# Kernel tuning notes

Measured on AMD Instinct MI355X. Metric: run time of the kernel, lower is better.

## Reference

```python
import jax, jax.numpy as jnp
import numpy as np

H_LSTM = 80          # span-encoder LSTM hidden
SPAN_DIM = 4 * H_LSTM  # 320
ADU_DIM = 256        # han_out_size
HEADS = 3
HAN_HID = 256
CTX_DIM = 200


def lstm(x, W_ih, W_hh, b, reverse=False):
    # x: [T, B, In] -> hidden states [T, B, H]; torch gate order i,f,g,o
    H = W_hh.shape[1]
    B = x.shape[1]

    def step(carry, xt):
        h, c = carry
        z = xt @ W_ih.T + h @ W_hh.T + b
        i, f, g, o = jnp.split(z, 4, axis=-1)
        c = jax.nn.sigmoid(f) * c + jax.nn.sigmoid(i) * jnp.tanh(g)
        h = jax.nn.sigmoid(o) * jnp.tanh(c)
        return (h, c), h

    init = (jnp.zeros((B, H), x.dtype), jnp.zeros((B, H), x.dtype))
    _, hs = jax.lax.scan(step, init, x, reverse=reverse)
    return hs


def span_rep(seq, spans):
    # seq [L, 2H], spans [..., 2] -> [..., 4H]
    f, bwd = seq[:, :H_LSTM], seq[:, H_LSTM:]
    i, j = spans[..., 0], spans[..., 1]
    fi1, fj = f[i - 1], f[j]
    bi, bj1 = bwd[i], bwd[j + 1]
    return jnp.concatenate([fj - fi1, bi - bj1, fi1, bj1], axis=-1)


def gat_metapath(h, src, dst, emask, W, a_l, a_r, bias):
    # single-metapath GATConv (dgl semantics): h [A, Din], W [K, Din, D]
    A = h.shape[0]
    hp = jnp.einsum('ad,kdo->ako', h, W)  # [A,K,D]
    e = jax.nn.leaky_relu(jnp.einsum('eko,ko->ek', hp[src], a_l)
                          + jnp.einsum('eko,ko->ek', hp[dst], a_r), 0.2)
    e = jnp.where(emask[:, None], e, -1e9)
    m = jax.ops.segment_max(e, dst, num_segments=A)           # [A,K]
    ex = jnp.where(emask[:, None], jnp.exp(e - m[dst]), 0.0)
    den = jax.ops.segment_sum(ex, dst, num_segments=A)
    alpha = ex / jnp.maximum(den[dst], 1e-9)                  # edge softmax per dst
    out = jax.ops.segment_sum(alpha[:, :, None] * hp[src], dst, num_segments=A)
    out = jax.nn.elu(out + bias)                              # [A,K,D]
    return out.reshape(A, -1)                                 # [A, K*D]


def attn_pool(feats, vals, mask, W1, b1, W2, b2):
    # tiny MLP -> Softmax over axis 0 over the kept (masked) set
    s = jnp.maximum(feats @ W1 + b1, 0.0) @ W2 + b2           # [N,1]
    s = jnp.where(mask[:, None], s, -1e9)
    a = jnp.where(mask[:, None], jax.nn.softmax(s, axis=0), 0.0)
    out = (a * vals).sum(0)
    return jnp.where(mask.any(), out, jnp.zeros_like(out))


def _forward(token_embed, info_scores,
             Wih_f, Whh_f, b_f, Wih_b, Whh_b, b_b,
             W_gat, a_l, a_r, b_gat, W_sem, b_sem, q_sem, W_pred, b_pred,
             W_adu1, b_adu1, W_adu2, b_adu2,
             W_inn1, b_inn1, W_inn2, b_inn2,
             W_int1, b_int1, W_int2, b_int2,
             Wih_c, Whh_c, b_c,
             comment_spans, adu_spans, adu_masks, local_masks,
             inner_src, inner_dst, inner_rel, inner_mask,
             inter_src, inter_dst, inter_rel, inter_mask):
    # bidirectional span encoder over frozen LF token embeddings
    x = token_embed.transpose(1, 0, 2)                        # [L, C, 768]
    hf = lstm(x, Wih_f, Whh_f, b_f)
    hb = lstm(x, Wih_b, Whh_b, b_b, reverse=True)
    span_enc = jnp.concatenate([hf, hb], -1).transpose(1, 0, 2)  # [C, L, 2H]

    def per_comment(seq, cspan, aspans, amask, lmask,
                    isrc, idst, irel, imask_e,
                    tsrc, tdst, trel, tmask_e, info):
        cemb = span_rep(seq, cspan)                           # [320]
        adus = span_rep(seq, aspans) * amask[:, None]         # [A, 320]
        A = adus.shape[0]
        # meta-paths: inner Attack, inner Support, inter AttackedBy(rev), inter SupportedBy(rev)
        srcs = jnp.stack([isrc, isrc, tdst, tdst])
        dsts = jnp.stack([idst, idst, tsrc, tsrc])
        masks = jnp.stack([imask_e & (irel == 0), imask_e & (irel == 1),
                           tmask_e & (trel == 0), tmask_e & (trel == 1)])
        z = jax.vmap(gat_metapath, in_axes=(None, 0, 0, 0, 0, 0, 0, 0))(
            adus, srcs, dsts, masks, W_gat, a_l, a_r, b_gat)  # [4, A, K*D]
        # semantic attention across meta-paths (masked mean over real nodes)
        w = jnp.tanh(z @ W_sem + b_sem) @ q_sem               # [4, A]
        w = (w * amask[None, :]).sum(1) / jnp.maximum(amask.sum(), 1)
        beta = jax.nn.softmax(w)                              # [4]
        zfin = jnp.einsum('m,mad->ad', beta, z)               # [A, K*D]
        adu_embeds = zfin @ W_pred + b_pred                   # [A, 256]
        # ADU attention pooling over locally-used ADUs
        feats = jnp.concatenate(
            [jnp.broadcast_to(cemb, (A, SPAN_DIM)), adu_embeds], -1)
        attended_adu = attn_pool(feats, adu_embeds, amask & lmask,
                                 W_adu1, b_adu1, W_adu2, b_adu2)

        def pair_attend(se, de, rel, me, W1, b1, W2, b2):
            # relation lut: Attack(0)->[0,1], Support(1)->[1,0]
            onehot = jnp.stack([rel, 1 - rel], -1).astype(adu_embeds.dtype)
            pe = jnp.concatenate([adu_embeds[se], adu_embeds[de], onehot], -1)  # [E,514]
            fp = jnp.concatenate(
                [jnp.broadcast_to(cemb, (pe.shape[0], SPAN_DIM)), pe], -1)
            return attn_pool(fp, pe, me, W1, b1, W2, b2)

        attended_inner = pair_attend(isrc, idst, irel, imask_e,
                                     W_inn1, b_inn1, W_inn2, b_inn2)
        # revert_inter_post_relations=True: embed = cat(emb[pair1], emb[pair0], rel)
        attended_inter = pair_attend(tdst, tsrc, trel, tmask_e,
                                     W_int1, b_int1, W_int2, b_int2)
        return jnp.concatenate([attended_adu, attended_inner, attended_inter,
                                info, cemb])                  # [1608]

    wo_ctx = jax.vmap(per_comment)(span_enc, comment_spans, adu_spans, adu_masks,
                                   local_masks, inner_src, inner_dst, inner_rel,
                                   inner_mask, inter_src, inter_dst, inter_rel,
                                   inter_mask, info_scores)   # [C, 1608]
    # comment compressor LSTM along the comment sequence (batch = 1)
    ctx = lstm(wo_ctx[:, None, :], Wih_c, Whh_c, b_c)[:, 0, :]  # [C, 200]
    return jnp.concatenate([ctx, wo_ctx], -1)                 # [C, 1808]


def setup_inputs():
    C, L, A, E, INFO = 64, 1024, 32, 48, 4
    key = jax.random.key(0)
    ks = iter(jax.random.split(key, 64))
    rng = np.random.default_rng(0)

    def u(shape):  # uniform init as in _weight_init, scaled for stability
        return jax.random.uniform(next(ks), shape, jnp.float32, -0.1, 0.1)

    token_embed = jax.random.normal(next(ks), (C, L, 768), jnp.float32)
    info_scores = jax.random.normal(next(ks), (C, INFO), jnp.float32)
    ci = rng.integers(1, L // 2, C)
    cj = rng.integers(L // 2, L - 2, C)
    comment_spans = jnp.stack([jnp.asarray(ci), jnp.asarray(cj)], 1).astype(jnp.int32)
    ai = rng.integers(1, L - 40, (C, A))
    adu_spans = jnp.stack([jnp.asarray(ai), jnp.asarray(ai + rng.integers(1, 30, (C, A)))], -1).astype(jnp.int32)
    adu_masks = jnp.ones((C, A), jnp.bool_)
    local_masks = jnp.asarray(rng.integers(0, 2, (C, A)) > 0)
    ei = lambda hi, shp: jnp.asarray(rng.integers(0, hi, shp), jnp.int32)
    eb = lambda shp: jnp.asarray(rng.integers(0, 2, shp) > 0)
    inp = dict(token_embed=token_embed, info_scores=info_scores,
               comment_spans=comment_spans, adu_spans=adu_spans,
               adu_masks=adu_masks, local_masks=local_masks,
               inner_src=ei(A, (C, E)), inner_dst=ei(A, (C, E)),
               inner_rel=ei(2, (C, E)), inner_mask=eb((C, E)),
               inter_src=ei(A, (C, E)), inter_dst=ei(A, (C, E)),
               inter_rel=ei(2, (C, E)), inter_mask=eb((C, E)))
    D_WO = SPAN_DIM + ADU_DIM * 5 + 4 + INFO  # 1608
    params = dict(
        Wih_f=u((4 * H_LSTM, 768)), Whh_f=u((4 * H_LSTM, H_LSTM)), b_f=u((4 * H_LSTM,)),
        Wih_b=u((4 * H_LSTM, 768)), Whh_b=u((4 * H_LSTM, H_LSTM)), b_b=u((4 * H_LSTM,)),
        W_gat=u((4, HEADS, SPAN_DIM, HAN_HID)), a_l=u((4, HEADS, HAN_HID)),
        a_r=u((4, HEADS, HAN_HID)), b_gat=u((4, HEADS, HAN_HID)),
        W_sem=u((HEADS * HAN_HID, 128)), b_sem=u((128,)), q_sem=u((128,)),
        W_pred=u((HEADS * HAN_HID, ADU_DIM)), b_pred=u((ADU_DIM,)),
        W_adu1=u((SPAN_DIM + ADU_DIM, 16)), b_adu1=u((16,)), W_adu2=u((16, 1)), b_adu2=u((1,)),
        W_inn1=u((SPAN_DIM + 2 * ADU_DIM + 2, 16)), b_inn1=u((16,)), W_inn2=u((16, 1)), b_inn2=u((1,)),
        W_int1=u((SPAN_DIM + 2 * ADU_DIM + 2, 16)), b_int1=u((16,)), W_int2=u((16, 1)), b_int2=u((1,)),
        Wih_c=u((4 * CTX_DIM, D_WO)), Whh_c=u((4 * CTX_DIM, CTX_DIM)), b_c=u((4 * CTX_DIM,)))
    inp.update(params)
    return inp


def reference(token_embed, info_scores,
              Wih_f, Whh_f, b_f, Wih_b, Whh_b, b_b,
              W_gat, a_l, a_r, b_gat, W_sem, b_sem, q_sem, W_pred, b_pred,
              W_adu1, b_adu1, W_adu2, b_adu2,
              W_inn1, b_inn1, W_inn2, b_inn2,
              W_int1, b_int1, W_int2, b_int2,
              Wih_c, Whh_c, b_c,
              comment_spans, adu_spans, adu_masks, local_masks,
              inner_src, inner_dst, inner_rel, inner_mask,
              inter_src, inter_dst, inter_rel, inter_mask):
    return _forward(token_embed, info_scores,
                    Wih_f, Whh_f, b_f, Wih_b, Whh_b, b_b,
                    W_gat, a_l, a_r, b_gat, W_sem, b_sem, q_sem, W_pred, b_pred,
                    W_adu1, b_adu1, W_adu2, b_adu2,
                    W_inn1, b_inn1, W_inn2, b_inn2,
                    W_int1, b_int1, W_int2, b_int2,
                    Wih_c, Whh_c, b_c,
                    comment_spans, adu_spans, adu_masks, local_masks,
                    inner_src, inner_dst, inner_rel, inner_mask,
                    inter_src, inter_dst, inter_rel, inter_mask)
```

## Files before the change

### kernel.cpp

```cpp
#include <hip/hip_runtime.h>
#include <hip/hip_bf16.h>
#include <hip/hip_fp16.h>
#include <stdint.h>

typedef unsigned int u32;
typedef unsigned short u16;
typedef __attribute__((ext_vector_type(8))) short short8;
typedef __attribute__((ext_vector_type(4))) float f32x4;
typedef _Float16 half2v __attribute__((ext_vector_type(2)));

#if defined(__has_builtin)
#if __has_builtin(__builtin_amdgcn_fdot2)
#define HAVE_FDOT2 1
#endif
#endif

#define LDS_BARRIER()                                        \
  do {                                                       \
    asm volatile("s_waitcnt lgkmcnt(0)" ::: "memory");       \
    __builtin_amdgcn_s_barrier();                            \
    asm volatile("" ::: "memory");                           \
  } while (0)

__device__ __forceinline__ float bf2f_u(u32 lo16) { return __uint_as_float(lo16 << 16); }
__device__ __forceinline__ u32 f2bf_bits(float x) {
  u32 u = __float_as_uint(x);
  return (u + 0x7fffu + ((u >> 16) & 1u)) >> 16;
}
__device__ __forceinline__ u32 pk2bf_tr(float x, float y) {
  return (__float_as_uint(y) & 0xffff0000u) | (__float_as_uint(x) >> 16);
}
__device__ __forceinline__ u32 pkh(float x, float y) {
  return (u32)__half_as_ushort(__float2half(x)) |
         ((u32)__half_as_ushort(__float2half(y)) << 16);
}
__device__ __forceinline__ float dot2h(u32 w, u32 h, float acc) {
#ifdef HAVE_FDOT2
  return __builtin_amdgcn_fdot2(__builtin_bit_cast(half2v, w), __builtin_bit_cast(half2v, h),
                                acc, false);
#else
  union { u32 u; __half2 h2; } uw, uh;
  uw.u = w; uh.u = h;
  float2 wf = __half22float2(uw.h2);
  float2 hf = __half22float2(uh.h2);
  return acc + wf.x * hf.x + wf.y * hf.y;
#endif
}
__device__ __forceinline__ float sigf(float x) { return 1.0f / (1.0f + __expf(-x)); }
__device__ __forceinline__ float tanhf_fast(float x) {
  float ax = fabsf(x);
  float e = __expf(-2.0f * ax);
  float t = (1.0f - e) / (1.0f + e);
  return x < 0.0f ? -t : t;
}
__device__ __forceinline__ float eluf(float x) { return x > 0.0f ? x : __expf(x) - 1.0f; }
__device__ __forceinline__ float lreluf(float x) { return x > 0.0f ? x : 0.2f * x; }

__device__ __forceinline__ int maskmode(const void* am) { return (*(const u32*)am) > 0xFFu; }
__device__ __forceinline__ int ldmask(const void* p, int i, int mb) {
  return mb ? (int)((const unsigned char*)p)[i] : ((const int*)p)[i];
}

__global__ void k_marker(float* out) { out[0] = 12345.0f; }

__global__ __launch_bounds__(256) void k_prep(const float* __restrict__ Wgat,
                                              const float* __restrict__ al,
                                              const float* __restrict__ ar,
                                              float* __restrict__ alproj,
                                              float* __restrict__ arproj) {
  int w = blockIdx.x * 4 + (threadIdx.x >> 6);
  int lane = threadIdx.x & 63;
  if (w >= 3840) return;
  int mk = w / 320, d = w % 320;
  const float* wrow = Wgat + ((size_t)mk * 320 + d) * 256;
  const float* alp = al + mk * 256;
  const float* arp = ar + mk * 256;
  float sa = 0.f, sb = 0.f;
#pragma unroll
  for (int q = 0; q < 4; ++q) {
    int o = lane + q * 64;
    float wv = wrow[o];
    sa += wv * alp[o];
    sb += wv * arp[o];
  }
#pragma unroll
  for (int off = 32; off; off >>= 1) {
    sa += __shfl_down(sa, off, 64);
    sb += __shfl_down(sb, off, 64);
  }
  if (lane == 0) { alproj[w] = sa; arproj[w] = sb; }
}

__global__ void k_pack(const float* __restrict__ whhc, uint4* __restrict__ wt4) {
  int idx = blockIdx.x * 256 + threadIdx.x;
  if (idx >= 20000) return;
  int k4 = idx / 800, r = idx % 800;
  const float* p = whhc + r * 200 + k4 * 8;
  wt4[idx] = (uint4){pkh(p[0], p[1]), pkh(p[2], p[3]), pkh(p[4], p[5]), pkh(p[6], p[7])};
}

__global__ __launch_bounds__(256) void k_gemm_in(
    const float* __restrict__ emb, const float* __restrict__ Wf, const float* __restrict__ Wb,
    const float* __restrict__ biasf, const float* __restrict__ biasb, float* __restrict__ Z) {
  __shared__ u16 Albs[128 * 40];
  __shared__ u16 Blbs[128 * 40];
  __shared__ float bias_l[128];
  const int tid = threadIdx.x;
  const int n0 = blockIdx.x * 128;
  const int m0 = blockIdx.y * 128;

  if (tid < 128) {
    int ng = n0 + tid;
    bias_l[tid] = (ng < 320) ? biasf[ng] : biasb[ng - 320];
  }
  const int srow = tid >> 1, shalf = tid & 1;
  const float* asrc = emb + (size_t)(m0 + srow) * 768 + shalf * 16;
  const int ngb = n0 + srow;
  const float* bsrc =
      ((ngb < 320) ? (Wf + (size_t)ngb * 768) : (Wb + (size_t)(ngb - 320) * 768)) + shalf * 16;
  u32* aw = (u32*)&Albs[srow * 40 + shalf * 16];
  u32* bw = (u32*)&Blbs[srow * 40 + shalf * 16];

  const int lane = tid & 63;
  const int lr = lane & 15, sub = lane >> 4;
  const int wv = tid >> 6, wm = wv >> 1, wn = wv & 1;
  const u16* abase = &Albs[(wm * 64 + lr) * 40 + sub * 8];
  const u16* bbase = &Blbs[(wn * 64 + lr) * 40 + sub * 8];

  f32x4 acc[4][4];
#pragma unroll
  for (int i = 0; i < 4; ++i)
#pragma unroll
    for (int j = 0; j < 4; ++j) acc[i][j] = (f32x4)(0.f);

  float4 a0, a1, a2, a3, b0, b1, b2, b3;
  u32 pra[8], prb[8];
  a0 = *(const float4*)(asrc + 0); a1 = *(const float4*)(asrc + 4);
  a2 = *(const float4*)(asrc + 8); a3 = *(const float4*)(asrc + 12);
  b0 = *(const float4*)(bsrc + 0); b1 = *(const float4*)(bsrc + 4);
  b2 = *(const float4*)(bsrc + 8); b3 = *(const float4*)(bsrc + 12);
  pra[0] = pk2bf_tr(a0.x, a0.y); pra[1] = pk2bf_tr(a0.z, a0.w);
  pra[2] = pk2bf_tr(a1.x, a1.y); pra[3] = pk2bf_tr(a1.z, a1.w);
  pra[4] = pk2bf_tr(a2.x, a2.y); pra[5] = pk2bf_tr(a2.z, a2.w);
  pra[6] = pk2bf_tr(a3.x, a3.y); pra[7] = pk2bf_tr(a3.z, a3.w);
  prb[0] = pk2bf_tr(b0.x, b0.y); prb[1] = pk2bf_tr(b0.z, b0.w);
  prb[2] = pk2bf_tr(b1.x, b1.y); prb[3] = pk2bf_tr(b1.z, b1.w);
  prb[4] = pk2bf_tr(b2.x, b2.y); prb[5] = pk2bf_tr(b2.z, b2.w);
  prb[6] = pk2bf_tr(b3.x, b3.y); prb[7] = pk2bf_tr(b3.z, b3.w);

  for (int it = 0; it < 24; ++it) {
    LDS_BARRIER();
#pragma unroll
    for (int q = 0; q < 8; ++q) { aw[q] = pra[q]; bw[q] = prb[q]; }
    LDS_BARRIER();
    const bool more = (it + 1 < 24);
    if (more) {
      const int k0 = (it + 1) * 32;
      a0 = *(const float4*)(asrc + k0); a1 = *(const float4*)(asrc + k0 + 4);
      a2 = *(const float4*)(asrc + k0 + 8); a3 = *(const float4*)(asrc + k0 + 12);
      b0 = *(const float4*)(bsrc + k0); b1 = *(const float4*)(bsrc + k0 + 4);
      b2 = *(const float4*)(bsrc + k0 + 8); b3 = *(const float4*)(bsrc + k0 + 12);
    }
    short8 bfr[4];
#pragma unroll
    for (int nf = 0; nf < 4; ++nf) bfr[nf] = *(const short8*)(bbase + nf * 640);
#pragma unroll
    for (int mf = 0; mf < 4; ++mf) {
      short8 af = *(const short8*)(abase + mf * 640);
#pragma unroll
      for (int nf = 0; nf < 4; ++nf)
        acc[mf][nf] = __builtin_amdgcn_mfma_f32_16x16x32_bf16(af, bfr[nf], acc[mf][nf], 0, 0, 0);
    }
    if (more) {
      pra[0] = pk2bf_tr(a0.x, a0.y); pra[1] = pk2bf_tr(a0.z, a0.w);
      pra[2] = pk2bf_tr(a1.x, a1.y); pra[3] = pk2bf_tr(a1.z, a1.w);
      pra[4] = pk2bf_tr(a2.x, a2.y); pra[5] = pk2bf_tr(a2.z, a2.w);
      pra[6] = pk2bf_tr(a3.x, a3.y); pra[7] = pk2bf_tr(a3.z, a3.w);
      prb[0] = pk2bf_tr(b0.x, b0.y); prb[1] = pk2bf_tr(b0.z, b0.w);
      prb[2] = pk2bf_tr(b1.x, b1.y); prb[3] = pk2bf_tr(b1.z, b1.w);
      prb[4] = pk2bf_tr(b2.x, b2.y); prb[5] = pk2bf_tr(b2.z, b2.w);
      prb[6] = pk2bf_tr(b3.x, b3.y); prb[7] = pk2bf_tr(b3.z, b3.w);
    }
  }
#pragma unroll
  for (int mf = 0; mf < 4; ++mf) {
#pragma unroll
    for (int nf = 0; nf < 4; ++nf) {
      int col = wn * 64 + nf * 16 + lr;
      float bias = bias_l[col];
      size_t mrow = (size_t)m0 + wm * 64 + mf * 16 + sub * 4;
#pragma unroll
      for (int j = 0; j < 4; ++j)
        Z[(mrow + j) * 640 + n0 + col] = acc[mf][nf][j] + bias;
    }
  }
}

__global__ __launch_bounds__(320, 1) void k_lstm_tok(const float* __restrict__ Z,
                                                     const float* __restrict__ Whhf,
                                                     const float* __restrict__ Whhb,
                                                     float* __restrict__ hf,
                                                     float* __restrict__ hb) {
  __shared__ uint2 wq[20 * 320];
  __shared__ alignas(16) u32 hpk[40];
  __shared__ float zbuf[320];
  const int tid = threadIdx.x;
  const int c = blockIdx.x >> 1;
  const int dir = blockIdx.x & 1;
  const float* Whh = dir ? Whhb : Whhf;
  float* hout = dir ? hb : hf;

  for (int idx = tid; idx < 20 * 320; idx += 320) {
    int k4 = idx / 320, r = idx % 320;
    const float* p = Whh + (size_t)r * 80 + k4 * 4;
    wq[idx] = (uint2){pkh(p[0], p[1]), pkh(p[2], p[3])};
  }
  if (tid < 40) hpk[tid] = 0;
  __syncthreads();

  const int j = tid;
  const bool isG = (j >= 160) && (j < 240);
  const uint2* wcol = wq + j;
  uint2 wv0 = wcol[0], wv1 = wcol[320], wv2 = wcol[640], wv3 = wcol[960];
  uint2 wv4 = wcol[1280], wv5 = wcol[1600], wv6 = wcol[1920], wv7 = wcol[2240];
  uint2 wv8 = wcol[2560], wv9 = wcol[2880], wv10 = wcol[3200], wv11 = wcol[3520];
  uint2 wv12 = wcol[3840], wv13 = wcol[4160], wv14 = wcol[4480], wv15 = wcol[4800];
  uint2 wv16 = wcol[5120], wv17 = wcol[5440], wv18 = wcol[5760], wv19 = wcol[6080];

  const int sgn = dir ? -1 : 1;
  const int t0 = dir ? 1023 : 0;
  const float* zb = Z + (size_t)c * 1024 * 640 + dir * 320 + j;
  float zc = zb[(size_t)t0 * 640];
  float zn = zb[(size_t)(t0 + sgn) * 640];
  float cst = 0.f;

  for (int t = 0; t < 1024; ++t) {
    const int tt = t0 + sgn * t;
    float zp = 0.f;
    if (t + 2 < 1024) zp = zb[(size_t)(t0 + sgn * (t + 2)) * 640];
    float a0 = zc, a1 = 0.f, a2 = 0.f, a3 = 0.f;
    {
      uint4 h0 = *(const uint4*)&hpk[0];
      a0 = dot2h(wv0.x, h0.x, a0); a1 = dot2h(wv0.y, h0.y, a1);
      a2 = dot2h(wv1.x, h0.z, a2); a3 = dot2h(wv1.y, h0.w, a3);
      uint4 h1 = *(const uint4*)&hpk[4];
      a0 = dot2h(wv2.x, h1.x, a0); a1 = dot2h(wv2.y, h1.y, a1);
      a2 = dot2h(wv3.x, h1.z, a2); a3 = dot2h(wv3.y, h1.w, a3);
      uint4 h2 = *(const uint4*)&hpk[8];
      a0 = dot2h(wv4.x, h2.x, a0); a1 = dot2h(wv4.y, h2.y, a1);
      a2 = dot2h(wv5.x, h2.z, a2); a3 = dot2h(wv5.y, h2.w, a3);
      uint4 h3 = *(const uint4*)&hpk[12];
      a0 = dot2h(wv6.x, h3.x, a0); a1 = dot2h(wv6.y, h3.y, a1);
      a2 = dot2h(wv7.x, h3.z, a2); a3 = dot2h(wv7.y, h3.w, a3);
      uint4 h4 = *(const uint4*)&hpk[16];
      a0 = dot2h(wv8.x, h4.x, a0); a1 = dot2h(wv8.y, h4.y, a1);
      a2 = dot2h(wv9.x, h4.z, a2); a3 = dot2h(wv9.y, h4.w, a3);
      uint4 h5 = *(const uint4*)&hpk[20];
      a0 = dot2h(wv10.x, h5.x, a0); a1 = dot2h(wv10.y, h5.y, a1);
      a2 = dot2h(wv11.x, h5.z, a2); a3 = dot2h(wv11.y, h5.w, a3);
      uint4 h6 = *(const uint4*)&hpk[24];
      a0 = dot2h(wv12.x, h6.x, a0); a1 = dot2h(wv12.y, h6.y, a1);
      a2 = dot2h(wv13.x, h6.z, a2); a3 = dot2h(wv13.y, h6.w, a3);
      uint4 h7 = *(const uint4*)&hpk[28];
      a0 = dot2h(wv14.x, h7.x, a0); a1 = dot2h(wv14.y, h7.y, a1);
      a2 = dot2h(wv15.x, h7.z, a2); a3 = dot2h(wv15.y, h7.w, a3);
      uint4 h8 = *(const uint4*)&hpk[32];
      a0 = dot2h(wv16.x, h8.x, a0); a1 = dot2h(wv16.y, h8.y, a1);
      a2 = dot2h(wv17.x, h8.z, a2); a3 = dot2h(wv17.y, h8.w, a3);
      uint4 h9 = *(const uint4*)&hpk[36];
      a0 = dot2h(wv18.x, h9.x, a0); a1 = dot2h(wv18.y, h9.y, a1);
      a2 = dot2h(wv19.x, h9.z, a2); a3 = dot2h(wv19.y, h9.w, a3);
    }
    float zr = (a0 + a1) + (a2 + a3);
    zbuf[j] = isG ? tanhf_fast(zr) : sigf(zr);
    LDS_BARRIER();
    if (j < 80) {
      float iv = zbuf[j];
      float fv = zbuf[80 + j];
      float gv = zbuf[160 + j];
      float ov = zbuf[240 + j];
      cst = fv * cst + iv * gv;
      float h = ov * tanhf_fast(cst);
      ((u16*)hpk)[j] = (u16)__half_as_ushort(__float2half(h));
      hout[((size_t)c * 1024 + tt) * 80 + j] = h;
    }
    zc = zn; zn = zp;
    LDS_BARRIER();
  }
}

__device__ __forceinline__ float span_val(const float* __restrict__ hf,
                                          const float* __restrict__ hb, int c, int i, int j,
                                          int d) {
  size_t base = (size_t)c * 1024 * 80;
  if (d < 80) return hf[base + (size_t)j * 80 + d] - hf[base + (size_t)(i - 1) * 80 + d];
  if (d < 160) return hb[base + (size_t)i * 80 + (d - 80)] - hb[base + (size_t)(j + 1) * 80 + (d - 80)];
  if (d < 240) return hf[base + (size_t)(i - 1) * 80 + (d - 160)];
  return hb[base + (size_t)(j + 1) * 80 + (d - 240)];
}

__global__ __launch_bounds__(256) void k_span(const float* __restrict__ hf,
                                              const float* __restrict__ hb,
                                              const int* __restrict__ cspan,
                                              const int* __restrict__ aspan,
                                              const void* __restrict__ amask,
                                              float* __restrict__ adus, float* __restrict__ cembo) {
  const int c = blockIdx.x, tid = threadIdx.x;
  const int mb = maskmode(amask);
  int ci = cspan[c * 2], cj = cspan[c * 2 + 1];
  for (int d = tid; d < 320; d += 256) cembo[c * 320 + d] = span_val(hf, hb, c, ci, cj, d);
  for (int idx = tid; idx < 32 * 320; idx += 256) {
    int a = idx / 320, d = idx % 320;
    float v = 0.f;
    if (ldmask(amask, c * 32 + a, mb)) {
      int ai = aspan[(c * 32 + a) * 2], aj = aspan[(c * 32 + a) * 2 + 1];
      v = span_val(hf, hb, c, ai, aj, d);
    }
    adus[(size_t)c * 10240 + idx] = v;
  }
}

__global__ __launch_bounds__(256) void k_gat(
    const float* __restrict__ adus_ws, const float* __restrict__ alproj,
    const float* __restrict__ arproj, const float* __restrict__ Wgat,
    const float* __restrict__ bgat, const int* __restrict__ isrc, const int* __restrict__ idst,
    const int* __restrict__ irel, const void* __restrict__ imask, const int* __restrict__ tsrc,
    const int* __restrict__ tdst, const int* __restrict__ trel, const void* __restrict__ tmask,
    const void* __restrict__ amdet, float* __restrict__ zgat) {
  __shared__ float adus_l[32][321];
  __shared__ float Wst[16][64];
  __shared__ float hp_t[32][66];
  __shared__ float sl_l[96], sr_l[96];
  __shared__ float e_l[144], alpha_l[144], mx_l[96], den_l[96];
  __shared__ int src_l[48], dst_l[48], valid_l[48];
  const int c = blockIdx.x >> 2, m = blockIdx.x & 3;
  const int tid = threadIdx.x;
  const int mb = maskmode(amdet);

  if (tid < 48) {
    int e = tid, s, d, r, mk;
    if (m < 2) {
      s = isrc[c * 48 + e]; d = idst[c * 48 + e]; r = irel[c * 48 + e];
      mk = ldmask(imask, c * 48 + e, mb);
    } else {
      s = tdst[c * 48 + e]; d = tsrc[c * 48 + e]; r = trel[c * 48 + e];
      mk = ldmask(tmask, c * 48 + e, mb);
    }
    src_l[e] = s; dst_l[e] = d; valid_l[e] = (mk != 0) && (r == (m & 1));
  }
  for (int idx = tid; idx < 32 * 320; idx += 256)
    adus_l[idx / 320][idx % 320] = adus_ws[(size_t)c * 10240 + idx];
  __syncthreads();

  if (tid < 96) {
    int a = tid & 31, k = tid >> 5;
    const float* alp = alproj + (m * 3 + k) * 320;
    const float* arp = arproj + (m * 3 + k) * 320;
    float sa = 0.f, sb = 0.f;
    for (int d = 0; d < 320; ++d) {
      float v = adus_l[a][d];
      sa += v * alp[d];
      sb += v * arp[d];
    }
    sl_l[a * 3 + k] = sa;
    sr_l[a * 3 + k] = sb;
  }
  __syncthreads();
  if (tid < 144) {
    int e = tid % 48, k = tid / 48;
    float v = -1e30f;
    if (valid_l[e]) v = lreluf(sl_l[src_l[e] * 3 + k] + sr_l[dst_l[e] * 3 + k]);
    e_l[e * 3 + k] = v;
  }
  __syncthreads();
  if (tid < 96) {
    int a = tid & 31, k = tid >> 5;
    float mx = -1e30f;
    for (int e = 0; e < 48; ++e)
      if (valid_l[e] && dst_l[e] == a) mx = fmaxf(mx, e_l[e * 3 + k]);
    float den = 0.f;
    for (int e = 0; e < 48; ++e)
      if (valid_l[e] && dst_l[e] == a) den += __expf(e_l[e * 3 + k] - mx);
    mx_l[a * 3 + k] = mx;
    den_l[a * 3 + k] = den;
  }
  __syncthreads();
  if (tid < 144) {
    int e = tid % 48, k = tid / 48;
    float v = 0.f;
    if (valid_l[e]) {
      int d = dst_l[e];
      v = __expf(e_l[e * 3 + k] - mx_l[d * 3 + k]) / fmaxf(den_l[d * 3 + k], 1e-9f);
    }
    alpha_l[e * 3 + k] = v;
  }
  __syncthreads();

  const int ag = tid >> 3, og = tid & 7;
  const int dd_ = tid >> 4, oq_ = (tid & 15) * 4;
  for (int k = 0; k < 3; ++k) {
    for (int ot = 0; ot < 4; ++ot) {
      float acc[8];
#pragma unroll
      for (int i = 0; i < 8; ++i) acc[i] = 0.f;
      float4 pref = *(const float4*)(Wgat + ((size_t)((m * 3 + k) * 320 + dd_)) * 256 + ot * 64 + oq_);
      for (int dt = 0; dt < 320; dt += 16) {
        Wst[dd_][oq_ + 0] = pref.x;
        Wst[dd_][oq_ + 1] = pref.y;
        Wst[dd_][oq_ + 2] = pref.z;
        Wst[dd_][oq_ + 3] = pref.w;
        __syncthreads();
        if (dt + 16 < 320)
          pref = *(const float4*)(Wgat +
                                  ((size_t)((m * 3 + k) * 320 + dt + 16 + dd_)) * 256 + ot * 64 + oq_);
#pragma unroll
        for (int dd = 0; dd < 16; ++dd) {
          float av = adus_l[ag][dt + dd];
          const float4 w0 = *(const float4*)(&Wst[dd][og * 8]);
          const float4 w1 = *(const float4*)(&Wst[dd][og * 8 + 4]);
          acc[0] += av * w0.x; acc[1] += av * w0.y; acc[2] += av * w0.z; acc[3] += av * w0.w;
          acc[4] += av * w1.x; acc[5] += av * w1.y; acc[6] += av * w1.z; acc[7] += av * w1.w;
        }
        __syncthreads();
      }
#pragma unroll
      for (int i = 0; i < 8; ++i) hp_t[ag][og * 8 + i] = acc[i];
      __syncthreads();
      float oacc[8];
#pragma unroll
      for (int i = 0; i < 8; ++i) oacc[i] = 0.f;
      for (int e = 0; e < 48; ++e) {
        if (valid_l[e] && dst_l[e] == ag) {
          float alv = alpha_l[e * 3 + k];
          int s = src_l[e];
#pragma unroll
          for (int i = 0; i < 8; ++i) oacc[i] += alv * hp_t[s][og * 8 + i];
        }
      }
#pragma unroll
      for (int i = 0; i < 8; ++i) {
        int o = ot * 64 + og * 8 + i;
        float v = eluf(oacc[i] + bgat[(m * 3 + k) * 256 + o]);
        zgat[((size_t)(c * 4 + m) * 32 + ag) * 768 + k * 256 + o] = v;
      }
      __syncthreads();
    }
  }
}

__global__ __launch_bounds__(256) void k_sem(const float* __restrict__ zgat,
                                             const float* __restrict__ Wsem,
                                             const float* __restrict__ bsem,
                                             const float* __restrict__ qsem,
                                             const void* __restrict__ amask,
                                             float* __restrict__ wsem) {
  __shared__ float Wst[64][128];
  __shared__ float zl[32][64];
  __shared__ float wred[256];
  __shared__ float war[32];
  const int c = blockIdx.x >> 2, m = blockIdx.x & 3;
  const int tid = threadIdx.x;
  const int mb = maskmode(amask);
  const int a = tid >> 3, hg = tid & 7;
  float acc[16];
#pragma unroll
  for (int i = 0; i < 16; ++i) acc[i] = 0.f;
  const float* zbase = zgat + (size_t)(c * 4 + m) * 32 * 768;
  for (int jt = 0; jt < 768; jt += 64) {
    for (int l = 0; l < 8; ++l) {
      int f4 = l * 256 + tid;
      int row = f4 >> 5, c4 = (f4 & 31) * 4;
      *(float4*)&Wst[row][c4] = *(const float4*)(Wsem + (size_t)(jt + row) * 128 + c4);
    }
    for (int l = 0; l < 2; ++l) {
      int f4 = l * 256 + tid;
      int row = f4 >> 4, c4 = (f4 & 15) * 4;
      *(float4*)&zl[row][c4] = *(const float4*)(zbase + (size_t)row * 768 + jt + c4);
    }
    __syncthreads();
    for (int j = 0; j < 64; ++j) {
      float zv = zl[a][j];
      const float* wp = &Wst[j][hg * 16];
#pragma unroll
      for (int i = 0; i < 16; ++i) acc[i] += zv * wp[i];
    }
    __syncthreads();
  }
  float wp_ = 0.f;
#pragma unroll
  for (int i = 0; i < 16; ++i) {
    int h = hg * 16 + i;
    wp_ += tanhf_fast(acc[i] + bsem[h]) * qsem[h];
  }
  wred[tid] = wp_;
  __syncthreads();
  if (tid < 32) {
    float s = 0.f;
    for (int q = 0; q < 8; ++q) s += wred[tid * 8 + q];
    war[tid] = s;
  }
  __syncthreads();
  if (tid == 0) {
    float s = 0.f;
    int cnt = 0;
    for (int aa = 0; aa < 32; ++aa)
      if (ldmask(amask, c * 32 + aa, mb)) { s += war[aa]; cnt++; }
    wsem[c * 4 + m] = s / (float)(cnt > 1 ? cnt : 1);
  }
}

__global__ __launch_bounds__(256) void k_comment(
    const float* __restrict__ zgat, const float* __restrict__ wsem,
    const float* __restrict__ cemb_ws, const float* __restrict__ Wpred,
    const float* __restrict__ bpred, const float* __restrict__ Wadu1,
    const float* __restrict__ badu1, const float* __restrict__ Wadu2,
    const float* __restrict__ badu2, const float* __restrict__ Winn1,
    const float* __restrict__ binn1, const float* __restrict__ Winn2,
    const float* __restrict__ binn2, const float* __restrict__ Wint1,
    const float* __restrict__ bint1, const float* __restrict__ Wint2,
    const float* __restrict__ bint2, const float* __restrict__ info,
    const void* __restrict__ amask, const void* __restrict__ lmask,
    const int* __restrict__ isrc, const int* __restrict__ idst,
    const int* __restrict__ irel, const void* __restrict__ imask, const int* __restrict__ tsrc,
    const int* __restrict__ tdst, const int* __restrict__ trel, const void* __restrict__ tmask,
    float* __restrict__ woctx, float* __restrict__ dout) {
  __shared__ float zf[32][133];
  __shared__ float ae[32][257];
  __shared__ float wbuf[13344];
  __shared__ float cemb_l[320];
  __shared__ float beta_l[4];
  __shared__ float pred_l[48][16];
  __shared__ float sE[48], alE[48];
  __shared__ int seL[48], deL[48], relL[48], mskL[48];
  __shared__ float wredA[256];
  __shared__ float sA[32], alA[32];
  __shared__ int mskA[32];
  const int c = blockIdx.x, tid = threadIdx.x;
  const int mb = maskmode(amask);

  if (tid == 0) {
    float w0 = wsem[c * 4], w1 = wsem[c * 4 + 1], w2 = wsem[c * 4 + 2], w3 = wsem[c * 4 + 3];
    float mx = fmaxf(fmaxf(w0, w1), fmaxf(w2, w3));
    float e0 = __expf(w0 - mx), e1 = __expf(w1 - mx), e2 = __expf(w2 - mx), e3 = __expf(w3 - mx);
    float s = e0 + e1 + e2 + e3;
    beta_l[0] = e0 / s; beta_l[1] = e1 / s; beta_l[2] = e2 / s; beta_l[3] = e3 / s;
  }
  for (int d = tid; d < 320; d += 256) cemb_l[d] = cemb_ws[c * 320 + d];
  __syncthreads();

  const int ag = tid >> 5;
  const int og = tid & 31;
  float acc[4][8];
#pragma unroll
  for (int i = 0; i < 4; ++i)
#pragma unroll
    for (int j = 0; j < 8; ++j) acc[i][j] = 0.f;
  const float b0 = beta_l[0], b1 = beta_l[1], b2 = beta_l[2], b3 = beta_l[3];
  const float* zc0 = zgat + (size_t)(c * 4 + 0) * 32 * 768;
  const float* zc1 = zgat + (size_t)(c * 4 + 1) * 32 * 768;
  const float* zc2 = zgat + (size_t)(c * 4 + 2) * 32 * 768;
  const float* zc3 = zgat + (size_t)(c * 4 + 3) * 32 * 768;
  for (int jt = 0; jt < 768; jt += 128) {
    for (int l = 0; l < 16; ++l) {
      int idx = l * 256 + tid;
      int a = idx >> 7, j = idx & 127;
      size_t off = (size_t)a * 768 + jt + j;
      zf[a][j] = b0 * zc0[off] + b1 * zc1[off] + b2 * zc2[off] + b3 * zc3[off];
    }
    __syncthreads();
    const float* wp0 = Wpred + (size_t)jt * 256 + og * 8;
    float4 w0v = *(const float4*)wp0;
    float4 w1v = *(const float4*)(wp0 + 4);
    for (int j = 0; j < 128; ++j) {
      float4 n0v, n1v;
      if (j + 1 < 128) {
        const float* wp = Wpred + (size_t)(jt + j + 1) * 256 + og * 8;
        n0v = *(const float4*)wp;
        n1v = *(const float4*)(wp + 4);
      }
      float w8[8] = {w0v.x, w0v.y, w0v.z, w0v.w, w1v.x, w1v.y, w1v.z, w1v.w};
      float z0 = zf[ag * 4 + 0][j], z1 = zf[ag * 4 + 1][j];
      float z2 = zf[ag * 4 + 2][j], z3 = zf[ag * 4 + 3][j];
#pragma unroll
      for (int jj = 0; jj < 8; ++jj) {
        acc[0][jj] += z0 * w8[jj];
        acc[1][jj] += z1 * w8[jj];
        acc[2][jj] += z2 * w8[jj];
        acc[3][jj] += z3 * w8[jj];
      }
      if (j + 1 < 128) { w0v = n0v; w1v = n1v; }
    }
    __syncthreads();
  }
#pragma unroll
  for (int i = 0; i < 4; ++i)
#pragma unroll
    for (int jj = 0; jj < 8; ++jj)
      ae[ag * 4 + i][og * 8 + jj] = acc[i][jj] + bpred[og * 8 + jj];
  for (int idx = tid; idx < 9216; idx += 256) wbuf[idx] = Wadu1[idx];
  __syncthreads();

  {
    const int a = tid >> 3, hg = tid & 7;
    float sacc = 0.f;
    for (int hh = 0; hh < 2; ++hh) {
      int h = hg * 2 + hh;
      float d = badu1[h];
      for (int dd = 0; dd < 320; ++dd) d += cemb_l[dd] * wbuf[dd * 16 + h];
      for (int dd = 0; dd < 256; ++dd) d += ae[a][dd] * wbuf[(320 + dd) * 16 + h];
      sacc += fmaxf(d, 0.f) * Wadu2[h];
    }
    wredA[tid] = sacc;
  }
  __syncthreads();
  if (tid < 32) {
    float s = badu2[0];
    for (int q = 0; q < 8; ++q) s += wredA[tid * 8 + q];
    sA[tid] = s;
    mskA[tid] = (ldmask(amask, c * 32 + tid, mb) != 0) && (ldmask(lmask, c * 32 + tid, mb) != 0);
  }
  __syncthreads();
  if (tid == 0) {
    float mx = -1e30f;
    int any = 0;
    for (int a = 0; a < 32; ++a)
      if (mskA[a]) { any = 1; mx = fmaxf(mx, sA[a]); }
    float s = 0.f;
    for (int a = 0; a < 32; ++a) {
      float v = mskA[a] ? __expf(sA[a] - mx) : 0.f;
      alA[a] = v;
      s += v;
    }
    if (any)
      for (int a = 0; a < 32; ++a) alA[a] /= s;
  }
  __syncthreads();
  {
    int o = tid;
    float v = 0.f;
    for (int a = 0; a < 32; ++a) v += alA[a] * ae[a][o];
    woctx[c * 1608 + o] = v;
    dout[(size_t)c * 1808 + 200 + o] = v;
  }
  __syncthreads();

  for (int pp = 0; pp < 2; ++pp) {
    const float *W1, *b1v, *W2, *b2v;
    const int *seP, *deP, *relP;
    const void* mskP;
    int outoff;
    if (pp == 0) {
      W1 = Winn1; b1v = binn1; W2 = Winn2; b2v = binn2;
      seP = isrc; deP = idst; relP = irel; mskP = imask; outoff = 256;
    } else {
      W1 = Wint1; b1v = bint1; W2 = Wint2; b2v = bint2;
      seP = tdst; deP = tsrc; relP = trel; mskP = tmask; outoff = 770;
    }
    if (tid < 48) {
      seL[tid] = seP[c * 48 + tid];
      deL[tid] = deP[c * 48 + tid];
      relL[tid] = relP[c * 48 + tid];
      mskL[tid] = (ldmask(mskP, c * 48 + tid, mb) != 0);
    }
    for (int idx = tid; idx < 13344; idx += 256) wbuf[idx] = W1[idx];
    __syncthreads();
    for (int u = tid; u < 768; u += 256) {
      int e = u >> 4, h = u & 15;
      int se = seL[e], de = deL[e];
      float rel = (float)relL[e];
      float d = b1v[h];
      for (int dd = 0; dd < 320; ++dd) d += cemb_l[dd] * wbuf[dd * 16 + h];
      for (int dd = 0; dd < 256; ++dd) d += ae[se][dd] * wbuf[(320 + dd) * 16 + h];
      for (int dd = 0; dd < 256; ++dd) d += ae[de][dd] * wbuf[(576 + dd) * 16 + h];
      d += rel * wbuf[832 * 16 + h] + (1.f - rel) * wbuf[833 * 16 + h];
      pred_l[e][h] = fmaxf(d, 0.f) * W2[h];
    }
    __syncthreads();
    if (tid < 48) {
      float s = b2v[0];
      for (int h = 0; h < 16; ++h) s += pred_l[tid][h];
      sE[tid] = s;
    }
    __syncthreads();
    if (tid == 0) {
      float mx = -1e30f;
      int any = 0;
      for (int e = 0; e < 48; ++e)
        if (mskL[e]) { any = 1; mx = fmaxf(mx, sE[e]); }
      float s = 0.f;
      for (int e = 0; e < 48; ++e) {
        float v = mskL[e] ? __expf(sE[e] - mx) : 0.f;
        alE[e] = v;
        s += v;
      }
      if (any)
        for (int e = 0; e < 48; ++e) alE[e] /= s;
    }
    __syncthreads();
    for (int dim = tid; dim < 514; dim += 256) {
      float v = 0.f;
      for (int e = 0; e < 48; ++e) {
        float alv = alE[e];
        float pe;
        if (dim < 256) pe = ae[seL[e]][dim];
        else if (dim < 512) pe = ae[deL[e]][dim - 256];
        else if (dim == 512) pe = (float)relL[e];
        else pe = 1.f - (float)relL[e];
        v += alv * pe;
      }
      woctx[c * 1608 + outoff + dim] = v;
      dout[(size_t)c * 1808 + 200 + outoff + dim] = v;
    }
    __syncthreads();
  }

  if (tid < 4) {
    float v = info[c * 4 + tid];
    woctx[c * 1608 + 1284 + tid] = v;
    dout[(size_t)c * 1808 + 200 + 1284 + tid] = v;
  }
  for (int d = tid; d < 320; d += 256) {
    float v = cemb_l[d];
    woctx[c * 1608 + 1288 + d] = v;
    dout[(size_t)c * 1808 + 200 + 1288 + d] = v;
  }
}

__global__ __launch_bounds__(256) void k_ctx_in(const float* __restrict__ woctx,
                                                const float* __restrict__ Wihc,
                                                const float* __restrict__ bc,
                                                float* __restrict__ xc) {
  __shared__ float woc[64][133];
  __shared__ float Wst[8][128];
  const int r0 = blockIdx.x * 8;
  const int tid = threadIdx.x;
  const int t = tid & 63, rg = tid >> 6;
  float a0 = 0.f, a1 = 0.f;
  for (int d0 = 0; d0 < 1608; d0 += 128) {
    int jn = 1608 - d0;
    if (jn > 128) jn = 128;
    for (int l = 0; l < 32; ++l) {
      int idx = l * 256 + tid;
      int tt = idx >> 7, j = idx & 127;
      woc[tt][j] = (j < jn) ? woctx[(size_t)tt * 1608 + d0 + j] : 0.f;
    }
    {
      int rr = tid >> 5, jb = tid & 31;
      for (int q = 0; q < 4; ++q) {
        int jj = jb * 4 + q;
        Wst[rr][jj] = (jj < jn) ? Wihc[(size_t)(r0 + rr) * 1608 + d0 + jj] : 0.f;
      }
    }
    __syncthreads();
    for (int j = 0; j < 128; ++j) {
      float x = woc[t][j];
      a0 += x * Wst[rg * 2 + 0][j];
      a1 += x * Wst[rg * 2 + 1][j];
    }
    __syncthreads();
  }
  int r = r0 + rg * 2;
  xc[t * 800 + r] = a0 + bc[r];
  xc[t * 800 + r + 1] = a1 + bc[r + 1];
}

__global__ __launch_bounds__(832) void k_ctx_rec(const float* __restrict__ xc,
                                                 const uint4* __restrict__ wt4,
                                                 float* __restrict__ dout) {
  __shared__ alignas(16) u32 hl2[100];
  __shared__ float zc[800];
  const int tid = threadIdx.x;
  if (tid < 100) hl2[tid] = 0;
  float cst = 0.f;
  __syncthreads();
  for (int t = 0; t < 64; ++t) {
    if (tid < 800) {
      float a0 = xc[t * 800 + tid], a1 = 0.f, a2 = 0.f, a3 = 0.f;
#pragma unroll 5
      for (int k4 = 0; k4 < 25; ++k4) {
        uint4 wv = wt4[(size_t)k4 * 800 + tid];
        uint4 hq = *(const uint4*)&hl2[k4 * 4];
        a0 = dot2h(wv.x, hq.x, a0);
        a1 = dot2h(wv.y, hq.y, a1);
        a2 = dot2h(wv.z, hq.z, a2);
        a3 = dot2h(wv.w, hq.w, a3);
      }
      zc[tid] = (a0 + a1) + (a2 + a3);
    }
    __syncthreads();
    if (tid < 200) {
      float iv = sigf(zc[tid]);
      float fv = sigf(zc[200 + tid]);
      float gv = tanhf_fast(zc[400 + tid]);
      float ov = sigf(zc[600 + tid]);
      cst = fv * cst + iv * gv;
      float h = ov * tanhf_fast(cst);
      ((u16*)hl2)[tid] = __half_as_ushort(__float2half(h));
      dout[(size_t)t * 1808 + tid] = h;
    }
    __syncthreads();
  }
}

extern "C" void kernel_launch(void* const* d_in, const int* in_sizes, int n_in, void* d_out,
                              int out_size, void* d_ws, size_t ws_size, hipStream_t stream) {
  const float* emb = (const float*)d_in[0];
  const float* info = (const float*)d_in[1];
  const int* cspan = (const int*)d_in[2];
  const int* aspan = (const int*)d_in[3];
  const void* amask = d_in[4];
  const void* lmask = d_in[5];
  const int* isrc = (const int*)d_in[6];
  const int* idst = (const int*)d_in[7];
  const int* irel = (const int*)d_in[8];
  const void* imask = d_in[9];
  const int* tsrc = (const int*)d_in[10];
  const int* tdst = (const int*)d_in[11];
  const int* trel = (const int*)d_in[12];
  const void* tmask = d_in[13];
  const float* Wihf = (const float*)d_in[14];
  const float* Whhf = (const float*)d_in[15];
  const float* bfv = (const float*)d_in[16];
  const float* Wihb = (const float*)d_in[17];
  const float* Whhb = (const float*)d_in[18];
  const float* bbv = (const float*)d_in[19];
  const float* Wgat = (const float*)d_in[20];
  const float* al = (const float*)d_in[21];
  const float* ar = (const float*)d_in[22];
  const float* bgat = (const float*)d_in[23];
  const float* Wsem = (const float*)d_in[24];
  const float* bsem = (const float*)d_in[25];
  const float* qsem = (const float*)d_in[26];
  const float* Wpred = (const float*)d_in[27];
  const float* bpred = (const float*)d_in[28];
  const float* Wadu1 = (const float*)d_in[29];
  const float* badu1 = (const float*)d_in[30];
  const float* Wadu2 = (const float*)d_in[31];
  const float* badu2 = (const float*)d_in[32];
  const float* Winn1 = (const float*)d_in[33];
  const float* binn1 = (const float*)d_in[34];
  const float* Winn2 = (const float*)d_in[35];
  const float* binn2 = (const float*)d_in[36];
  const float* Wint1 = (const float*)d_in[37];
  const float* bint1 = (const float*)d_in[38];
  const float* Wint2 = (const float*)d_in[39];
  const float* bint2 = (const float*)d_in[40];
  const float* Wihc = (const float*)d_in[41];
  const float* Whhc = (const float*)d_in[42];
  const float* bc = (const float*)d_in[43];
  float* out = (float*)d_out;
  float* ws = (float*)d_ws;

  const size_t OFF_Z = 0;
  const size_t OFF_HF = OFF_Z + (size_t)65536 * 640;
  const size_t OFF_HB = OFF_HF + (size_t)64 * 1024 * 80;
  const size_t OFF_ZG = OFF_HB + (size_t)64 * 1024 * 80;
  const size_t OFF_AD = OFF_ZG + (size_t)64 * 4 * 32 * 768;
  const size_t OFF_CE = OFF_AD + (size_t)64 * 32 * 320;
  const size_t OFF_WS4 = OFF_CE + 64 * 320;
  const size_t OFF_ALP = OFF_WS4 + 256;
  const size_t OFF_ARP = OFF_ALP + 3840;
  const size_t OFF_WO = OFF_ARP + 3840;
  const size_t OFF_XC = OFF_WO + (size_t)64 * 1608;
  const size_t OFF_WT = OFF_XC + (size_t)64 * 800;
  const size_t TOTAL = OFF_WT + 80000;

  if (n_in < 44 || ws_size < TOTAL * sizeof(float)) {
    k_marker<<<1, 1, 0, stream>>>(out);
    return;
  }

  k_prep<<<960, 256, 0, stream>>>(Wgat, al, ar, ws + OFF_ALP, ws + OFF_ARP);
  k_pack<<<79, 256, 0, stream>>>(Whhc, (uint4*)(ws + OFF_WT));
  dim3 g1(5, 512);
  k_gemm_in<<<g1, 256, 0, stream>>>(emb, Wihf, Wihb, bfv, bbv, ws + OFF_Z);
  k_lstm_tok<<<128, 320, 0, stream>>>(ws + OFF_Z, Whhf, Whhb, ws + OFF_HF, ws + OFF_HB);
  k_span<<<64, 256, 0, stream>>>(ws + OFF_HF, ws + OFF_HB, cspan, aspan, amask, ws + OFF_AD,
                                 ws + OFF_CE);
  k_gat<<<256, 256, 0, stream>>>(ws + OFF_AD, ws + OFF_ALP, ws + OFF_ARP, Wgat, bgat, isrc, idst,
                                 irel, imask, tsrc, tdst, trel, tmask, amask, ws + OFF_ZG);
  k_sem<<<256, 256, 0, stream>>>(ws + OFF_ZG, Wsem, bsem, qsem, amask, ws + OFF_WS4);
  k_comment<<<64, 256, 0, stream>>>(ws + OFF_ZG, ws + OFF_WS4, ws + OFF_CE, Wpred, bpred, Wadu1,
                                    badu1, Wadu2, badu2, Winn1, binn1, Winn2, binn2, Wint1, bint1,
                                    Wint2, bint2, info, amask, lmask, isrc, idst, irel, imask,
                                    tsrc, tdst, trel, tmask, ws + OFF_WO, out);
  k_ctx_in<<<100, 256, 0, stream>>>(ws + OFF_WO, Wihc, bc, ws + OFF_XC);
  k_ctx_rec<<<1, 832, 0, stream>>>(ws + OFF_XC, (const uint4*)(ws + OFF_WT), out);
}
```

Baseline: 1.576 ms.

## Interleave LSTM gates per quad and exchange via swizzle to drop a barrier

The token LSTM kernel now remaps weight columns so each group of four adjacent lanes holds the i, f, g and o gates of one hidden unit. The gates are exchanged with ds_swizzle quad broadcasts instead of an LDS buffer, which removes one block barrier per timestep. The hidden state is double-buffered by step parity. A single exp-based formula (tanh written as 2*sigmoid(2x)-1) replaces the divergent sigmoid/tanh branch. The cell update is now computed redundantly on all 320 lanes rather than 80, and the fused activation formula may differ slightly in numerics.

New measurement: 1.599 ms. About the same (+1.5%).

```diff
diff --git a/kernel.cpp b/kernel.cpp
--- a/kernel.cpp
+++ b/kernel.cpp
@@ -202,8 +202,7 @@
                                                      float* __restrict__ hf,
                                                      float* __restrict__ hb) {
   __shared__ uint2 wq[20 * 320];
-  __shared__ alignas(16) u32 hpk[40];
-  __shared__ float zbuf[320];
+  __shared__ alignas(16) u32 hpk[80];
   const int tid = threadIdx.x;
   const int c = blockIdx.x >> 1;
   const int dir = blockIdx.x & 1;
@@ -211,16 +210,24 @@
   float* hout = dir ? hb : hf;
 
   for (int idx = tid; idx < 20 * 320; idx += 320) {
-    int k4 = idx / 320, r = idx % 320;
-    const float* p = Whh + (size_t)r * 80 + k4 * 4;
+    int k4 = idx / 320, cpos = idx % 320;
+    int row = (cpos & 3) * 80 + (cpos >> 2);
+    const float* p = Whh + (size_t)row * 80 + k4 * 4;
     wq[idx] = (uint2){pkh(p[0], p[1]), pkh(p[2], p[3])};
   }
-  if (tid < 40) hpk[tid] = 0;
-  __syncthreads();
-
-  const int j = tid;
-  const bool isG = (j >= 160) && (j < 240);
-  const uint2* wcol = wq + j;
+  if (tid < 80) hpk[tid] = 0;
+  __syncthreads();
+
+  const int g = tid & 3;
+  const int m = tid >> 2;
+  const int r = g * 80 + m;
+  const bool isG = (g == 2);
+  const bool isLead = (g == 0);
+  const float zrMul = isG ? 2.0f : 1.0f;
+  const float actMul = isG ? 2.0f : 1.0f;
+  const float actAdd = isG ? -1.0f : 0.0f;
+
+  const uint2* wcol = wq + tid;
   uint2 wv0 = wcol[0], wv1 = wcol[320], wv2 = wcol[640], wv3 = wcol[960];
   uint2 wv4 = wcol[1280], wv5 = wcol[1600], wv6 = wcol[1920], wv7 = wcol[2240];
   uint2 wv8 = wcol[2560], wv9 = wcol[2880], wv10 = wcol[3200], wv11 = wcol[3520];
@@ -229,7 +236,7 @@
 
   const int sgn = dir ? -1 : 1;
   const int t0 = dir ? 1023 : 0;
-  const float* zb = Z + (size_t)c * 1024 * 640 + dir * 320 + j;
+  const float* zb = Z + (size_t)c * 1024 * 640 + dir * 320 + r;
   float zc = zb[(size_t)t0 * 640];
   float zn = zb[(size_t)(t0 + sgn) * 640];
   float cst = 0.f;
@@ -238,51 +245,56 @@
     const int tt = t0 + sgn * t;
     float zp = 0.f;
     if (t + 2 < 1024) zp = zb[(size_t)(t0 + sgn * (t + 2)) * 640];
+    const int par = t & 1;
+    const uint4* hread = (const uint4*)(hpk + (par ^ 1) * 40);
     float a0 = zc, a1 = 0.f, a2 = 0.f, a3 = 0.f;
     {
-      uint4 h0 = *(const uint4*)&hpk[0];
+      uint4 h0 = hread[0];
       a0 = dot2h(wv0.x, h0.x, a0); a1 = dot2h(wv0.y, h0.y, a1);
       a2 = dot2h(wv1.x, h0.z, a2); a3 = dot2h(wv1.y, h0.w, a3);
-      uint4 h1 = *(const uint4*)&hpk[4];
+      uint4 h1 = hread[1];
       a0 = dot2h(wv2.x, h1.x, a0); a1 = dot2h(wv2.y, h1.y, a1);
       a2 = dot2h(wv3.x, h1.z, a2); a3 = dot2h(wv3.y, h1.w, a3);
-      uint4 h2 = *(const uint4*)&hpk[8];
+      uint4 h2 = hread[2];
       a0 = dot2h(wv4.x, h2.x, a0); a1 = dot2h(wv4.y, h2.y, a1);
       a2 = dot2h(wv5.x, h2.z, a2); a3 = dot2h(wv5.y, h2.w, a3);
-      uint4 h3 = *(const uint4*)&hpk[12];
+      uint4 h3 = hread[3];
       a0 = dot2h(wv6.x, h3.x, a0); a1 = dot2h(wv6.y, h3.y, a1);
       a2 = dot2h(wv7.x, h3.z, a2); a3 = dot2h(wv7.y, h3.w, a3);
-      uint4 h4 = *(const uint4*)&hpk[16];
+      uint4 h4 = hread[4];
       a0 = dot2h(wv8.x, h4.x, a0); a1 = dot2h(wv8.y, h4.y, a1);
       a2 = dot2h(wv9.x, h4.z, a2); a3 = dot2h(wv9.y, h4.w, a3);
-      uint4 h5 = *(const uint4*)&hpk[20];
+      uint4 h5 = hread[5];
       a0 = dot2h(wv10.x, h5.x, a0); a1 = dot2h(wv10.y, h5.y, a1);
       a2 = dot2h(wv11.x, h5.z, a2); a3 = dot2h(wv11.y, h5.w, a3);
-      uint4 h6 = *(const uint4*)&hpk[24];
+      uint4 h6 = hread[6];
       a0 = dot2h(wv12.x, h6.x, a0); a1 = dot2h(wv12.y, h6.y, a1);
       a2 = dot2h(wv13.x, h6.z, a2); a3 = dot2h(wv13.y, h6.w, a3);
-      uint4 h7 = *(const uint4*)&hpk[28];
+      uint4 h7 = hread[7];
       a0 = dot2h(wv14.x, h7.x, a0); a1 = dot2h(wv14.y, h7.y, a1);
       a2 = dot2h(wv15.x, h7.z, a2); a3 = dot2h(wv15.y, h7.w, a3);
-      uint4 h8 = *(const uint4*)&hpk[32];
+      uint4 h8 = hread[8];
       a0 = dot2h(wv16.x, h8.x, a0); a1 = dot2h(wv16.y, h8.y, a1);
       a2 = dot2h(wv17.x, h8.z, a2); a3 = dot2h(wv17.y, h8.w, a3);
-      uint4 h9 = *(const uint4*)&hpk[36];
+      uint4 h9 = hread[9];
       a0 = dot2h(wv18.x, h9.x, a0); a1 = dot2h(wv18.y, h9.y, a1);
       a2 = dot2h(wv19.x, h9.z, a2); a3 = dot2h(wv19.y, h9.w, a3);
     }
     float zr = (a0 + a1) + (a2 + a3);
-    zbuf[j] = isG ? tanhf_fast(zr) : sigf(zr);
-    LDS_BARRIER();
-    if (j < 80) {
-      float iv = zbuf[j];
-      float fv = zbuf[80 + j];
-      float gv = zbuf[160 + j];
-      float ov = zbuf[240 + j];
-      cst = fv * cst + iv * gv;
-      float h = ov * tanhf_fast(cst);
-      ((u16*)hpk)[j] = (u16)__half_as_ushort(__float2half(h));
-      hout[((size_t)c * 1024 + tt) * 80 + j] = h;
+    float xs = zr * zrMul;
+    float e = __expf(fminf(-xs, 80.0f));
+    float sg = 1.0f / (1.0f + e);
+    float act = sg * actMul + actAdd;
+    u32 au = __float_as_uint(act);
+    float iv = __uint_as_float(__builtin_amdgcn_ds_swizzle(au, 0x8000));
+    float fv = __uint_as_float(__builtin_amdgcn_ds_swizzle(au, 0x8055));
+    float gv = __uint_as_float(__builtin_amdgcn_ds_swizzle(au, 0x80AA));
+    float ov = __uint_as_float(__builtin_amdgcn_ds_swizzle(au, 0x80FF));
+    cst = fv * cst + iv * gv;
+    float h = ov * tanhf_fast(cst);
+    if (isLead) {
+      ((u16*)(hpk + par * 40))[m] = (u16)__half_as_ushort(__float2half(h));
+      hout[((size_t)c * 1024 + tt) * 80 + m] = h;
     }
     zc = zn; zn = zp;
     LDS_BARRIER();
```
